# Optimization experiments

Measured on AMD Instinct MI355X. Metric: run time of the kernel, lower is better.

The kernel has to match this reference:

```python
import jax, jax.numpy as jnp
import numpy as np

NODE, HIDDEN, BATCH, OUT, BUF = 200, 10, 50, 64, 500
DT = 0.0001
# ParamsJR('JR') defaults (all variances 0 -> constants, not Parameters)
A_, a_, B_, b_ = 3.25, 100.0, 22.0, 50.0
g_, c1_, c2_, c3_, c4_ = 1000.0, 135.0, 135.0 * 0.8, 135.0 * 0.25, 135.0 * 0.25
std_in_, vmax, v0, r_, y0, cy0 = 100.0, 5.0, 6.0, 0.56, 2.0, 5.0
LB, U_UB, NOISE_LB, SAT = 0.01, 500.0, 150.0, 1000.0


def setup_inputs() -> dict:
    key = jax.random.key(0)
    ks = jax.random.split(key, 8)
    inp = jax.random.normal(ks[0], (NODE, HIDDEN, BATCH), dtype=jnp.float32)
    noise_in = jax.random.normal(ks[1], (NODE, HIDDEN, BATCH), dtype=jnp.float32)
    hx = jax.random.uniform(ks[2], (NODE, 6), dtype=jnp.float32)
    hE = jax.random.uniform(ks[3], (NODE, BUF), dtype=jnp.float32)
    sc = jax.random.uniform(ks[4], (NODE, NODE), dtype=jnp.float32)
    w_bb = jax.random.uniform(ks[5], (NODE, NODE), dtype=jnp.float32)  # fitted gains (init 0.05 in torch)
    lm = jax.random.normal(ks[6], (OUT, NODE), dtype=jnp.float32)  # lead-field
    delays = jax.random.randint(ks[7], (NODE, NODE), 0, BUF)  # (dist/(1.5+relu(mu))).int64
    return {"inp": inp, "noise_in": noise_in, "hx": hx, "hE": hE,
            "sc": sc, "w_bb": w_bb, "lm": lm, "delays": delays}


def _sigmoid(x):
    return vmax / (1.0 + jnp.exp(r_ * (v0 - x)))


def _sys2nd(A, a, u, x, v):
    return A * a * u - 2.0 * a * v - a * a * x


def _forward(inp, noise_in, hx, hE, sc, w_bb, lm, delays):
    relu = jax.nn.relu
    A_e, a_e = relu(A_), 1.0 + relu(a_)          # 0*con+relu(A), 1*con+relu(a)
    B_e, b_e = relu(B_), 1.0 + relu(b_)
    g_e, c1e, c2e, c3e, c4e = (LB + relu(g_), LB + relu(c1_), LB + relu(c2_),
                               LB + relu(c3_), LB + relu(c4_))
    std_e = NOISE_LB + relu(std_in_)

    # normalized laplacian-style connectivity
    w = jnp.exp(w_bb) * sc
    wl = jnp.log1p(0.5 * (w + w.T))
    w_n = wl / jnp.linalg.norm(wl)
    dg = -jnp.diag(jnp.sum(w_n, axis=1))          # (node, node)
    rows = jnp.arange(NODE)[:, None]

    def step(carry, xs):
        M, E, I, Mv, Ev, Iv, hEb = carry
        u, noise = xs                              # (node,1) each
        Ed = hEb[rows, delays]                     # Ed[i,j] = hE[i, delays[i,j]]
        LEd = jnp.sum(w_n * Ed.T, axis=1, keepdims=True)  # (node,1)
        rM = _sigmoid(E - I)
        rE = (std_e * noise + g_e * (LEd + dg @ E)
              + c2e * _sigmoid(c1e * M))
        rI = c4e * _sigmoid(c3e * M)
        ddM = M + DT * Mv
        ddE = E + DT * Ev
        ddI = I + DT * Iv
        ddMv = Mv + DT * _sys2nd(A_e, a_e, u + U_UB * jnp.tanh(rM / U_UB), M, Mv)
        ddEv = Ev + DT * _sys2nd(A_e, a_e, U_UB * jnp.tanh(rE / U_UB), E, Ev)
        ddIv = Iv + DT * _sys2nd(B_e, b_e, U_UB * jnp.tanh(rI / U_UB), I, Iv)
        sat = lambda x: SAT * jnp.tanh(x / SAT)
        M, E, I, Mv, Ev, Iv = (sat(ddM), sat(ddE), sat(ddI),
                               sat(ddMv), sat(ddEv), sat(ddIv))
        hEb = jnp.concatenate([M, hEb[:, :-1]], axis=1)  # push pyramidal state into delay buffer
        return (M, E, I, Mv, Ev, Iv, hEb), None

    def tr_step(carry, xs):
        u_tr, n_tr = xs                            # (hidden, node, 1)
        carry, _ = jax.lax.scan(step, carry, (u_tr, n_tr))
        M, E, I, Mv, Ev, Iv, _ = carry
        return carry, (M[:, 0], E[:, 0], I[:, 0], Mv[:, 0], Ev[:, 0], Iv[:, 0])

    M, E, I = hx[:, 0:1], hx[:, 1:2], hx[:, 2:3]
    Mv, Ev, Iv = hx[:, 3:4], hx[:, 4:5], hx[:, 5:6]
    u_all = jnp.transpose(inp, (2, 1, 0))[..., None]       # (batch, hidden, node, 1)
    n_all = jnp.transpose(noise_in, (2, 1, 0))[..., None]
    carry, recs = jax.lax.scan(tr_step, (M, E, I, Mv, Ev, Iv, hE), (u_all, n_all))
    Mb, Eb, Ib, Mvb, Evb, Ivb = recs                       # (batch, node) each

    # lead-field: row-normalize then remove channel mean
    lm_n = lm / jnp.sqrt(jnp.sum(lm ** 2, axis=1, keepdims=True))
    lm_t = lm_n - jnp.mean(lm_n, axis=0, keepdims=True)
    eeg = cy0 * jnp.einsum('on,bn->ob', lm_t, Eb - Ib) - y0  # (output, batch)

    M, E, I, Mv, Ev, Iv, hEb = carry
    current_state = jnp.concatenate([M, E, I, Mv, Ev, Iv], axis=1)
    return eeg, current_state, Eb.T, Ib.T, Mb.T, Evb.T, Ivb.T, Mvb.T, hEb


def reference(inp, noise_in, hx, hE, sc, w_bb, lm, delays):
    return _forward(inp, noise_in, hx, hE, sc, w_bb, lm, delays)
```

## Files before the change

kernel.cpp:

```cpp
#include <hip/hip_runtime.h>
#include <math.h>

#define N_NODE 200
#define RING   512
#define ROWF   545
#define NSTEP  500
#define TB     32
#define NB     16
#define NWG    8
#define NTHR   256
#define JSL    25
#define NEARCAP 32
#define MDEP   36

#define FPBUF   (NWG * N_NODE * TB)
#define OFF_FP  0
#define OFF_BAR (2 * FPBUF)
#define WS_NEED ((size_t)(2 * FPBUF + 64) * 4)

#define SM_RED   0
#define SM_MREC  64
#define SM_US    28864
#define SM_NS    54464
#define SM_LED   80864
#define SM_RING  106464
#define SM_TOTAL 160964
#define SM_LMT   64
#define SM_DIFF  51264

__device__ __forceinline__ float ftanh(float x) {
    float ax = fabsf(x);
    float t  = __expf(-2.0f * ax);
    float r  = __fdividef(1.0f - t, 1.0f + t);
    return copysignf(r, x);
}
__device__ __forceinline__ float sigm(float x) {
    return __fdividef(5.0f, 1.0f + __expf(0.56f * (6.0f - x)));
}
__device__ __forceinline__ float satf(float x) {
    return 1000.0f * ftanh(x * 0.001f);
}

__device__ __forceinline__ void grid_barrier(int* slot, int nwg) {
    __syncthreads();
    if (threadIdx.x == 0) {
        __threadfence();
        __hip_atomic_fetch_add(slot, 1, __ATOMIC_ACQ_REL, __HIP_MEMORY_SCOPE_AGENT);
        while (__hip_atomic_load(slot, __ATOMIC_ACQUIRE, __HIP_MEMORY_SCOPE_AGENT) < nwg) {
            __builtin_amdgcn_s_sleep(2);
        }
        __threadfence();
    }
    __syncthreads();
}

__global__ void zero_bar(int* bar) {
    if (threadIdx.x < 64) bar[threadIdx.x] = 0;
}

__global__ __launch_bounds__(NTHR, 1)
void jansen_fast(const float* __restrict__ inp, const float* __restrict__ noise_in,
                 const float* __restrict__ hx,  const float* __restrict__ hE,
                 const float* __restrict__ sc,  const float* __restrict__ wbb,
                 const float* __restrict__ lm,  const int*   __restrict__ delays,
                 float* __restrict__ out, float* __restrict__ ws)
{
    __shared__ char smem[SM_TOTAL];
    double*   red  = (double*)(smem + SM_RED);
    float*    Mrec = (float*)(smem + SM_MREC);
    unsigned* nOFF = (unsigned*)(smem + SM_US);
    float*    nW   = (float*)(smem + SM_NS);
    float*    uS   = (float*)(smem + SM_US);
    float*    nS   = (float*)(smem + SM_NS);
    float*    LEdS = (float*)(smem + SM_LED);
    float*    ringS= (float*)(smem + SM_RING);

    const int tid = threadIdx.x;
    const int wg  = blockIdx.x;
    const int i   = tid;
    const int jlo = wg * JSL;

    float* fp  = ws + OFF_FP;
    int*   bar = (int*)(ws + OFF_BAR);

    double ssq = 0.0;
    for (int q = tid; q < N_NODE * N_NODE; q += NTHR) {
        int j = q / N_NODE, ii = q - j * N_NODE;
        float w1 = expf(wbb[ii * N_NODE + j]) * sc[ii * N_NODE + j];
        float w2 = expf(wbb[j * N_NODE + ii]) * sc[j * N_NODE + ii];
        float wl = log1pf(0.5f * (w1 + w2));
        ssq += (double)wl * (double)wl;
    }
    #pragma unroll
    for (int off = 32; off > 0; off >>= 1) ssq += __shfl_down(ssq, off, 64);
    if ((tid & 63) == 0) red[tid >> 6] = ssq;

    for (int p = tid; p < JSL * ROWF; p += NTHR) {
        int jl = p / ROWF, x = p - jl * ROWF;
        float v = 0.0f;
        if (x < 544) {
            int dd = (x < RING) ? (511 - x) : (1023 - x);
            if (dd < 500) v = hE[(jlo + jl) * 500 + dd];
        }
        ringS[p] = v;
    }
    for (int p = tid; p < MDEP * N_NODE; p += NTHR) {
        int s = p / N_NODE, j = p - s * N_NODE;
        Mrec[p] = (s >= 4) ? hE[j * 500 + (35 - s)] : 0.0f;
    }
    for (int p = tid; p < NEARCAP * N_NODE; p += NTHR) {
        nOFF[p] = 0u;
        nW[p]   = 0.0f;
    }
    __syncthreads();
    if (tid == 0) {
        double s = 0.0;
        #pragma unroll
        for (int r = 0; r < 8; ++r) s += red[r];
        red[0] = 1.0 / sqrt(s);
    }
    __syncthreads();
    const float inv = (float)red[0];

    float rowsum = 0.0f;
    float M = 0, E = 0, I = 0, Mvv = 0, Evv = 0, Ivv = 0;
    float wreg[JSL];
    int   ereg[JSL];
    #pragma unroll
    for (int jl = 0; jl < JSL; ++jl) { wreg[jl] = 0.0f; ereg[jl] = 0; }
    if (i < N_NODE) {
        int cnt = 0;
        for (int j = 0; j < N_NODE; ++j) {
            float w1 = expf(wbb[i * N_NODE + j]) * sc[i * N_NODE + j];
            float w2 = expf(wbb[j * N_NODE + i]) * sc[j * N_NODE + i];
            float w  = log1pf(0.5f * (w1 + w2)) * inv;
            int d = delays[j * N_NODE + i];
            rowsum += w;
            if (d < NEARCAP && cnt < NEARCAP) {
                nOFF[cnt * N_NODE + i] = (unsigned)((35 - d) * N_NODE + j);
                nW  [cnt * N_NODE + i] = w;
                ++cnt;
            }
        }
        #pragma unroll
        for (int jl = 0; jl < JSL; ++jl) {
            int j = jlo + jl;
            float w1 = expf(wbb[i * N_NODE + j]) * sc[i * N_NODE + j];
            float w2 = expf(wbb[j * N_NODE + i]) * sc[j * N_NODE + i];
            float w  = log1pf(0.5f * (w1 + w2)) * inv;
            int d = delays[j * N_NODE + i];
            wreg[jl] = (d < NEARCAP) ? 0.0f : w;
            ereg[jl] = 511 - d;
        }
        M   = hx[i * 6 + 0]; E   = hx[i * 6 + 1]; I   = hx[i * 6 + 2];
        Mvv = hx[i * 6 + 3]; Evv = hx[i * 6 + 4]; Ivv = hx[i * 6 + 5];
    }

    int   noffR[NEARCAP];
    float nwR[NEARCAP];
    {
        const int ii = (i < N_NODE) ? i : 0;
        #pragma unroll
        for (int n = 0; n < NEARCAP; ++n) {
            noffR[n] = (int)nOFF[n * N_NODE + ii];
            nwR[n]   = nW[n * N_NODE + ii];
        }
    }
    __syncthreads();

    for (int b = 0; b < NB; ++b) {
        const int t0 = b * TB;
        float* fpb = fp + (b & 1) * FPBUF;

        if (i < N_NODE) {
            float ac[TB];
            #pragma unroll
            for (int k = 0; k < TB; ++k) ac[k] = 0.0f;
            #pragma unroll
            for (int jl = 0; jl < JSL; ++jl) {
                float w  = wreg[jl];
                int   p0 = (t0 + ereg[jl]) & 511;
                const float* rb = ringS + jl * ROWF + p0;
                #pragma unroll
                for (int k = 0; k < TB; ++k)
                    ac[k] = fmaf(w, rb[k], ac[k]);
            }
            float4* fpw = (float4*)(fpb + wg * (N_NODE * TB) + i * TB);
            #pragma unroll
            for (int q = 0; q < 8; ++q)
                fpw[q] = make_float4(ac[4*q+0], ac[4*q+1], ac[4*q+2], ac[4*q+3]);

            #pragma unroll
            for (int k = 0; k < TB; ++k) {
                int t = t0 + k;
                float uv = 0.0f, nv = 0.0f;
                if (t < NSTEP) {
                    int bb = t / 10, h = t - 10 * bb;
                    uv = inp     [i * 500 + h * 50 + bb];
                    nv = noise_in[i * 500 + h * 50 + bb];
                }
                uS[k * N_NODE + i] = uv;
                nS[k * N_NODE + i] = nv;
            }
        }

        grid_barrier(bar + b, NWG);

        if (i < N_NODE) {
            const float* basep = fpb + i * TB;
            #pragma unroll
            for (int c = 0; c < 8; ++c) {
                float sx = 0, sy = 0, sz = 0, sw = 0;
                #pragma unroll
                for (int g = 0; g < NWG; ++g) {
                    float4 q = *(const float4*)(basep + g * (N_NODE * TB) + c * 4);
                    sx += q.x; sy += q.y; sz += q.z; sw += q.w;
                }
                LEdS[(c * 4 + 0) * N_NODE + i] = sx;
                LEdS[(c * 4 + 1) * N_NODE + i] = sy;
                LEdS[(c * 4 + 2) * N_NODE + i] = sz;
                LEdS[(c * 4 + 3) * N_NODE + i] = sw;
            }
        }
        __syncthreads();

        const int kmax = (NSTEP - t0 < TB) ? (NSTEP - t0) : TB;
        int s36 = t0 % MDEP;
        int bcur = t0 / 10, hcur = t0 - 10 * bcur;
        const bool ringw = (i >= jlo) && (i < jlo + JSL);
        const int  rbase = (i - jlo) * ROWF;
        for (int k = 0; k < kmax; ++k) {
            const int t = t0 + k;
            if (i < N_NODE) {
                const int base36 = s36 * N_NODE;
                float a0 = LEdS[k * N_NODE + i];
                float a1 = 0.0f, a2 = 0.0f, a3 = 0.0f;
                #pragma unroll
                for (int n = 0; n < NEARCAP; n += 4) {
                    int d0 = base36 + noffR[n+0]; if (d0 >= MDEP*N_NODE) d0 -= MDEP*N_NODE;
                    int d1 = base36 + noffR[n+1]; if (d1 >= MDEP*N_NODE) d1 -= MDEP*N_NODE;
                    int d2 = base36 + noffR[n+2]; if (d2 >= MDEP*N_NODE) d2 -= MDEP*N_NODE;
                    int d3 = base36 + noffR[n+3]; if (d3 >= MDEP*N_NODE) d3 -= MDEP*N_NODE;
                    a0 = fmaf(nwR[n+0], Mrec[d0], a0);
                    a1 = fmaf(nwR[n+1], Mrec[d1], a1);
                    a2 = fmaf(nwR[n+2], Mrec[d2], a2);
                    a3 = fmaf(nwR[n+3], Mrec[d3], a3);
                }
                float LEd = (a0 + a1) + (a2 + a3);
                float u  = uS[k * N_NODE + i];
                float nz = nS[k * N_NODE + i];
                float rM = sigm(E - I);
                float rE = 250.0f * nz + 1000.01f * (LEd - rowsum * E) + 108.01f * sigm(135.01f * M);
                float rI = 33.76f * sigm(33.76f * M);
                float ddM = M + 1e-4f * Mvv;
                float ddE = E + 1e-4f * Evv;
                float ddI = I + 1e-4f * Ivv;
                float uu  = u + 500.0f * ftanh(rM * 0.002f);
                float ddMv = Mvv + 1e-4f * (328.25f * uu - 202.0f * Mvv - 10201.0f * M);
                float uE  = 500.0f * ftanh(rE * 0.002f);
                float ddEv = Evv + 1e-4f * (328.25f * uE - 202.0f * Evv - 10201.0f * E);
                float uI  = 500.0f * ftanh(rI * 0.002f);
                float ddIv = Ivv + 1e-4f * (1122.0f * uI - 102.0f * Ivv - 2601.0f * I);
                M   = satf(ddM);  E   = satf(ddE);  I   = satf(ddI);
                Mvv = satf(ddMv); Evv = satf(ddEv); Ivv = satf(ddIv);
                Mrec[base36 + i] = M;
                if (ringw) {
                    int pt = t & 511;
                    ringS[rbase + pt] = M;
                    if (pt < 32) ringS[rbase + pt + 512] = M;
                }
                if (wg == 0 && hcur == 9) {
                    out[ 4400 + i * 50 + bcur] = E;
                    out[14400 + i * 50 + bcur] = I;
                    out[24400 + i * 50 + bcur] = M;
                    out[34400 + i * 50 + bcur] = Evv;
                    out[44400 + i * 50 + bcur] = Ivv;
                    out[54400 + i * 50 + bcur] = Mvv;
                }
                ++hcur; if (hcur == 10) { hcur = 0; ++bcur; }
                ++s36; if (s36 == MDEP) s36 = 0;
            }
            __syncthreads();
        }
    }

    for (int p = tid; p < JSL * 500; p += NTHR) {
        int jl = p / 500, dd = p - jl * 500;
        out[64400 + (jlo + jl) * 500 + dd] = ringS[jl * ROWF + ((499 - dd) & 511)];
    }
    if (wg != 0) return;

    if (i < N_NODE) {
        out[3200 + i * 6 + 0] = M;
        out[3200 + i * 6 + 1] = E;
        out[3200 + i * 6 + 2] = I;
        out[3200 + i * 6 + 3] = Mvv;
        out[3200 + i * 6 + 4] = Evv;
        out[3200 + i * 6 + 5] = Ivv;
    }

    float* lmt  = (float*)(smem + SM_LMT);
    float* diff = (float*)(smem + SM_DIFF);
    __syncthreads();
    if (tid < 64) {
        float s = 0.0f;
        for (int n = 0; n < N_NODE; ++n) { float v = lm[tid * N_NODE + n]; s += v * v; }
        float ivn = 1.0f / sqrtf(s);
        for (int n = 0; n < N_NODE; ++n) lmt[tid * N_NODE + n] = lm[tid * N_NODE + n] * ivn;
    }
    __syncthreads();
    if (tid < N_NODE) {
        float s = 0.0f;
        for (int o = 0; o < 64; ++o) s += lmt[o * N_NODE + tid];
        s *= (1.0f / 64.0f);
        for (int o = 0; o < 64; ++o) lmt[o * N_NODE + tid] -= s;
    }
    __syncthreads();
    for (int p = tid; p < 10000; p += NTHR) diff[p] = out[4400 + p] - out[14400 + p];
    __syncthreads();
    for (int p = tid; p < 3200; p += NTHR) {
        int o = p / 50, bb = p - o * 50;
        float s = 0.0f;
        for (int n = 0; n < N_NODE; ++n)
            s = fmaf(lmt[o * N_NODE + n], diff[n * 50 + bb], s);
        out[p] = 5.0f * s - 2.0f;
    }
}

__global__ __launch_bounds__(1024, 1)
void jansen_main(const float* __restrict__ inp, const float* __restrict__ noise_in,
                 const float* __restrict__ hx,  const float* __restrict__ hE,
                 const float* __restrict__ sc,  const float* __restrict__ wbb,
                 const float* __restrict__ lm,  const int*   __restrict__ delays,
                 float* __restrict__ out, float* __restrict__ ws)
{
    const int tid = threadIdx.x;
    const int i   = tid & 255;
    const int c   = tid >> 8;

    float* ring = ws;
    float* lmt  = ws + N_NODE * RING;

    __shared__ double red[18];
    __shared__ float  part[4][N_NODE];
    __shared__ float  wn[N_NODE * N_NODE];

    double ssq = 0.0;
    for (int p = tid; p < N_NODE * N_NODE; p += 1024) {
        int r0 = p / N_NODE;
        int cc = p - r0 * N_NODE;
        float w1 = expf(wbb[p]) * sc[p];
        float w2 = expf(wbb[cc * N_NODE + r0]) * sc[cc * N_NODE + r0];
        float v  = log1pf(0.5f * (w1 + w2));
        wn[p] = v;
        ssq += (double)v * (double)v;
    }
    #pragma unroll
    for (int off = 32; off > 0; off >>= 1) ssq += __shfl_down(ssq, off, 64);
    if ((tid & 63) == 0) red[tid >> 6] = ssq;
    __syncthreads();
    if (tid == 0) {
        double s = 0.0;
        for (int k = 0; k < 16; ++k) s += red[k];
        red[16] = 1.0 / sqrt(s);
    }
    __syncthreads();
    const float inv_norm = (float)red[16];
    for (int p = tid; p < N_NODE * N_NODE; p += 1024) wn[p] *= inv_norm;

    for (int p = tid; p < N_NODE * 500; p += 1024) {
        int j = p / 500, dd = p - j * 500;
        ring[j * RING + (511 - dd)] = hE[p];
    }
    if (tid < 64) {
        float s = 0.0f;
        for (int n = 0; n < N_NODE; ++n) { float v = lm[tid * N_NODE + n]; s += v * v; }
        float inv = 1.0f / sqrtf(s);
        for (int n = 0; n < N_NODE; ++n) lmt[tid * N_NODE + n] = lm[tid * N_NODE + n] * inv;
    }
    __syncthreads();
    if (tid < N_NODE) {
        float s = 0.0f;
        for (int o = 0; o < 64; ++o) s += lmt[o * N_NODE + tid];
        s *= (1.0f / 64.0f);
        for (int o = 0; o < 64; ++o) lmt[o * N_NODE + tid] -= s;
    }

    unsigned int dpk[25];
    if (i < N_NODE) {
        #pragma unroll
        for (int r0 = 0; r0 < 25; ++r0) {
            int d0 = delays[(c * 50 + 2 * r0    ) * N_NODE + i];
            int d1 = delays[(c * 50 + 2 * r0 + 1) * N_NODE + i];
            unsigned e0 = (unsigned)((-1 - d0) & 511);
            unsigned e1 = (unsigned)((-1 - d1) & 511);
            dpk[r0] = e0 | (e1 << 16);
        }
    }

    float M = 0, E = 0, I = 0, Mvv = 0, Evv = 0, Ivv = 0, rowsum = 0;
    if (c == 0 && i < N_NODE) {
        M   = hx[i * 6 + 0]; E   = hx[i * 6 + 1]; I   = hx[i * 6 + 2];
        Mvv = hx[i * 6 + 3]; Evv = hx[i * 6 + 4]; Ivv = hx[i * 6 + 5];
    }
    __syncthreads();
    if (c == 0 && i < N_NODE) {
        float s = 0.0f;
        for (int j = 0; j < N_NODE; ++j) s += wn[j * N_NODE + i];
        rowsum = s;
    }

    for (int t = 0; t < NSTEP; ++t) {
        if (i < N_NODE) {
            float acc = 0.0f;
            const float* ringc = ring + c * 50 * RING;
            const float* wnc   = wn + c * 50 * N_NODE + i;
            #pragma unroll
            for (int r0 = 0; r0 < 50; ++r0) {
                unsigned e = (dpk[r0 >> 1] >> ((r0 & 1) << 4)) & 0xffffu;
                int pos = (int)(((unsigned)t + e) & 511u);
                acc = fmaf(wnc[r0 * N_NODE], ringc[r0 * RING + pos], acc);
            }
            part[c][i] = acc;
        }
        __syncthreads();
        if (c == 0 && i < N_NODE) {
            float LEd = part[0][i] + part[1][i] + part[2][i] + part[3][i];
            int b = t / 10, h = t - b * 10;
            float u  = inp     [i * 500 + h * 50 + b];
            float nz = noise_in[i * 500 + h * 50 + b];
            float rM = 5.0f / (1.0f + expf(0.56f * (6.0f - (E - I))));
            float rE = 250.0f * nz + 1000.01f * (LEd - rowsum * E) + 108.01f * (5.0f / (1.0f + expf(0.56f * (6.0f - 135.01f * M))));
            float rI = 33.76f * (5.0f / (1.0f + expf(0.56f * (6.0f - 33.76f * M))));
            float ddM = M + 1e-4f * Mvv;
            float ddE = E + 1e-4f * Evv;
            float ddI = I + 1e-4f * Ivv;
            float uu  = u + 500.0f * tanhf(rM / 500.0f);
            float ddMv = Mvv + 1e-4f * (328.25f * uu - 202.0f * Mvv - 10201.0f * M);
            float uE  = 500.0f * tanhf(rE / 500.0f);
            float ddEv = Evv + 1e-4f * (328.25f * uE - 202.0f * Evv - 10201.0f * E);
            float uI  = 500.0f * tanhf(rI / 500.0f);
            float ddIv = Ivv + 1e-4f * (1122.0f * uI - 102.0f * Ivv - 2601.0f * I);
            M   = 1000.0f * tanhf(ddM / 1000.0f);
            E   = 1000.0f * tanhf(ddE / 1000.0f);
            I   = 1000.0f * tanhf(ddI / 1000.0f);
            Mvv = 1000.0f * tanhf(ddMv / 1000.0f);
            Evv = 1000.0f * tanhf(ddEv / 1000.0f);
            Ivv = 1000.0f * tanhf(ddIv / 1000.0f);
            ring[i * RING + (t & 511)] = M;
            if (h == 9) {
                out[ 4400 + i * 50 + b] = E;
                out[14400 + i * 50 + b] = I;
                out[24400 + i * 50 + b] = M;
                out[34400 + i * 50 + b] = Evv;
                out[44400 + i * 50 + b] = Ivv;
                out[54400 + i * 50 + b] = Mvv;
            }
        }
        __syncthreads();
    }

    if (c == 0 && i < N_NODE) {
        out[3200 + i * 6 + 0] = M;
        out[3200 + i * 6 + 1] = E;
        out[3200 + i * 6 + 2] = I;
        out[3200 + i * 6 + 3] = Mvv;
        out[3200 + i * 6 + 4] = Evv;
        out[3200 + i * 6 + 5] = Ivv;
    }
    for (int p = tid; p < N_NODE * 500; p += 1024) {
        int ii = p / 500, dd = p - ii * 500;
        out[64400 + p] = ring[ii * RING + (499 - dd)];
    }
    __syncthreads();
    for (int p = tid; p < 64 * 50; p += 1024) {
        int o = p / 50, b = p - o * 50;
        float s = 0.0f;
        for (int n = 0; n < N_NODE; ++n)
            s += lmt[o * N_NODE + n] * (out[4400 + n * 50 + b] - out[14400 + n * 50 + b]);
        out[p] = 5.0f * s - 2.0f;
    }
}

extern "C" void kernel_launch(void* const* d_in, const int* in_sizes, int n_in,
                              void* d_out, int out_size, void* d_ws, size_t ws_size,
                              hipStream_t stream) {
    if (ws_size >= WS_NEED) {
        zero_bar<<<1, 64, 0, stream>>>((int*)((float*)d_ws + OFF_BAR));
        jansen_fast<<<NWG, NTHR, 0, stream>>>(
            (const float*)d_in[0], (const float*)d_in[1], (const float*)d_in[2],
            (const float*)d_in[3], (const float*)d_in[4], (const float*)d_in[5],
            (const float*)d_in[6], (const int*)d_in[7],
            (float*)d_out, (float*)d_ws);
    } else {
        jansen_main<<<1, 1024, 0, stream>>>(
            (const float*)d_in[0], (const float*)d_in[1], (const float*)d_in[2],
            (const float*)d_in[3], (const float*)d_in[4], (const float*)d_in[5],
            (const float*)d_in[6], (const int*)d_in[7],
            (float*)d_out, (float*)d_ws);
    }
}
```

Baseline: 1.210 ms.

## Run sequential inner recurrence in a single wavefront with four nodes per lane

The per-step recurrence is moved from 200 threads synchronised with __syncthreads every step to one 64-lane wavefront, where each lane owns four nodes and the block barriers inside the time loop are dropped. The near-delay window shrinks from 32 to 16 steps, so more connections go through the blocked far-field accumulation, and the time block is halved from 32 to 16 steps, which doubles the number of grid barriers. Near-neighbour sums use variable-length chunks based on per-node counts. The intent is to remove per-step workgroup barrier cost at the expense of four times more serial arithmetic per lane.

```diff
diff --git a/kernel.cpp b/kernel.cpp
--- a/kernel.cpp
+++ b/kernel.cpp
@@ -3,15 +3,17 @@
 
 #define N_NODE 200
 #define RING   512
-#define ROWF   545
+#define ROWF   527
 #define NSTEP  500
-#define TB     32
-#define NB     16
+#define TB     16
+#define NB     32
 #define NWG    8
 #define NTHR   256
 #define JSL    25
-#define NEARCAP 32
-#define MDEP   36
+#define NEARB  16
+#define NCAP   24
+#define MDEP   20
+#define MSZ    (MDEP * N_NODE)
 
 #define FPBUF   (NWG * N_NODE * TB)
 #define OFF_FP  0
@@ -20,11 +22,14 @@
 
 #define SM_RED   0
 #define SM_MREC  64
-#define SM_US    28864
-#define SM_NS    54464
-#define SM_LED   80864
-#define SM_RING  106464
-#define SM_TOTAL 160964
+#define SM_LEDS  16064
+#define SM_UN    28864
+#define SM_NCNT  54464
+#define SM_ST    55264
+#define SM_RING  91264
+#define SM_TOTAL 143964
+#define SM_NX    16064
+#define SM_NW2   35264
 #define SM_LMT   64
 #define SM_DIFF  51264
 
@@ -59,21 +64,22 @@
 }
 
 __global__ __launch_bounds__(NTHR, 1)
-void jansen_fast(const float* __restrict__ inp, const float* __restrict__ noise_in,
-                 const float* __restrict__ hx,  const float* __restrict__ hE,
-                 const float* __restrict__ sc,  const float* __restrict__ wbb,
-                 const float* __restrict__ lm,  const int*   __restrict__ delays,
-                 float* __restrict__ out, float* __restrict__ ws)
+void jansen_1w(const float* __restrict__ inp, const float* __restrict__ noise_in,
+               const float* __restrict__ hx,  const float* __restrict__ hE,
+               const float* __restrict__ sc,  const float* __restrict__ wbb,
+               const float* __restrict__ lm,  const int*   __restrict__ delays,
+               float* __restrict__ out, float* __restrict__ ws)
 {
     __shared__ char smem[SM_TOTAL];
     double*   red  = (double*)(smem + SM_RED);
-    float*    Mrec = (float*)(smem + SM_MREC);
-    unsigned* nOFF = (unsigned*)(smem + SM_US);
-    float*    nW   = (float*)(smem + SM_NS);
-    float*    uS   = (float*)(smem + SM_US);
-    float*    nS   = (float*)(smem + SM_NS);
-    float*    LEdS = (float*)(smem + SM_LED);
+    float*    MrecF= (float*)(smem + SM_MREC);
+    float*    LEdS = (float*)(smem + SM_LEDS);
+    float*    unF  = (float*)(smem + SM_UN);
+    unsigned* nCnt = (unsigned*)(smem + SM_NCNT);
+    float*    stS  = (float*)(smem + SM_ST);
     float*    ringS= (float*)(smem + SM_RING);
+    unsigned* nX   = (unsigned*)(smem + SM_NX);
+    float*    nW2  = (float*)(smem + SM_NW2);
 
     const int tid = threadIdx.x;
     const int wg  = blockIdx.x;
@@ -97,38 +103,28 @@
 
     for (int p = tid; p < JSL * ROWF; p += NTHR) {
         int jl = p / ROWF, x = p - jl * ROWF;
-        float v = 0.0f;
-        if (x < 544) {
-            int dd = (x < RING) ? (511 - x) : (1023 - x);
-            if (dd < 500) v = hE[(jlo + jl) * 500 + dd];
-        }
-        ringS[p] = v;
-    }
-    for (int p = tid; p < MDEP * N_NODE; p += NTHR) {
+        int dd = (x < RING) ? (511 - x) : (1023 - x);
+        ringS[p] = (dd < 500) ? hE[(jlo + jl) * 500 + dd] : 0.0f;
+    }
+    for (int p = tid; p < MSZ; p += NTHR) {
         int s = p / N_NODE, j = p - s * N_NODE;
-        Mrec[p] = (s >= 4) ? hE[j * 500 + (35 - s)] : 0.0f;
-    }
-    for (int p = tid; p < NEARCAP * N_NODE; p += NTHR) {
-        nOFF[p] = 0u;
-        nW[p]   = 0.0f;
-    }
+        MrecF[p] = (s >= 4) ? hE[j * 500 + (19 - s)] : 0.0f;
+    }
+    for (int p = tid; p < NCAP * N_NODE; p += NTHR) { nX[p] = 0u; nW2[p] = 0.0f; }
     __syncthreads();
     if (tid == 0) {
-        double s = 0.0;
-        #pragma unroll
-        for (int r = 0; r < 8; ++r) s += red[r];
+        double s = red[0] + red[1] + red[2] + red[3];
         red[0] = 1.0 / sqrt(s);
     }
     __syncthreads();
     const float inv = (float)red[0];
 
-    float rowsum = 0.0f;
-    float M = 0, E = 0, I = 0, Mvv = 0, Evv = 0, Ivv = 0;
     float wreg[JSL];
     int   ereg[JSL];
     #pragma unroll
     for (int jl = 0; jl < JSL; ++jl) { wreg[jl] = 0.0f; ereg[jl] = 0; }
     if (i < N_NODE) {
+        float rowsum = 0.0f;
         int cnt = 0;
         for (int j = 0; j < N_NODE; ++j) {
             float w1 = expf(wbb[i * N_NODE + j]) * sc[i * N_NODE + j];
@@ -136,12 +132,13 @@
             float w  = log1pf(0.5f * (w1 + w2)) * inv;
             int d = delays[j * N_NODE + i];
             rowsum += w;
-            if (d < NEARCAP && cnt < NEARCAP) {
-                nOFF[cnt * N_NODE + i] = (unsigned)((35 - d) * N_NODE + j);
-                nW  [cnt * N_NODE + i] = w;
+            if (d < NEARB && cnt < NCAP) {
+                nX [cnt * N_NODE + i] = (unsigned)((19 - d) * N_NODE + j);
+                nW2[cnt * N_NODE + i] = w;
                 ++cnt;
             }
         }
+        nCnt[i] = (unsigned)cnt;
         #pragma unroll
         for (int jl = 0; jl < JSL; ++jl) {
             int j = jlo + jl;
@@ -149,22 +146,53 @@
             float w2 = expf(wbb[j * N_NODE + i]) * sc[j * N_NODE + i];
             float w  = log1pf(0.5f * (w1 + w2)) * inv;
             int d = delays[j * N_NODE + i];
-            wreg[jl] = (d < NEARCAP) ? 0.0f : w;
+            wreg[jl] = (d < NEARB) ? 0.0f : w;
             ereg[jl] = 511 - d;
         }
-        M   = hx[i * 6 + 0]; E   = hx[i * 6 + 1]; I   = hx[i * 6 + 2];
-        Mvv = hx[i * 6 + 3]; Evv = hx[i * 6 + 4]; Ivv = hx[i * 6 + 5];
-    }
-
-    int   noffR[NEARCAP];
-    float nwR[NEARCAP];
-    {
-        const int ii = (i < N_NODE) ? i : 0;
+        stS[0 * N_NODE + i] = hx[i * 6 + 0];
+        stS[1 * N_NODE + i] = hx[i * 6 + 1];
+        stS[2 * N_NODE + i] = hx[i * 6 + 2];
+        stS[3 * N_NODE + i] = hx[i * 6 + 3];
+        stS[4 * N_NODE + i] = hx[i * 6 + 4];
+        stS[5 * N_NODE + i] = hx[i * 6 + 5];
+        stS[6 * N_NODE + i] = rowsum;
+    }
+    __syncthreads();
+
+    const int  nb        = tid * 4;
+    const bool innerLane = (tid < 64) && (nb < N_NODE);
+    int   pkA[4 * NCAP]; float wkA[4 * NCAP];
+    int   cq[4];
+    float Mq[4] = {0,0,0,0}, Eq[4] = {0,0,0,0}, Iq[4] = {0,0,0,0};
+    float Mvq[4] = {0,0,0,0}, Evq[4] = {0,0,0,0}, Ivq[4] = {0,0,0,0};
+    float rsq[4] = {0,0,0,0};
+    #pragma unroll
+    for (int z = 0; z < 4 * NCAP; ++z) { pkA[z] = 0; wkA[z] = 0.0f; }
+    cq[0] = cq[1] = cq[2] = cq[3] = 0;
+    if (innerLane) {
         #pragma unroll
-        for (int n = 0; n < NEARCAP; ++n) {
-            noffR[n] = (int)nOFF[n * N_NODE + ii];
-            nwR[n]   = nW[n * N_NODE + ii];
-        }
+        for (int q = 0; q < 4; ++q) {
+            cq[q] = (int)nCnt[nb + q];
+            #pragma unroll
+            for (int n = 0; n < NCAP; ++n) {
+                pkA[q * NCAP + n] = (int)nX[n * N_NODE + nb + q];
+                wkA[q * NCAP + n] = nW2[n * N_NODE + nb + q];
+            }
+        }
+        float4 v0 = *(const float4*)(stS + 0 * N_NODE + nb);
+        float4 v1 = *(const float4*)(stS + 1 * N_NODE + nb);
+        float4 v2 = *(const float4*)(stS + 2 * N_NODE + nb);
+        float4 v3 = *(const float4*)(stS + 3 * N_NODE + nb);
+        float4 v4 = *(const float4*)(stS + 4 * N_NODE + nb);
+        float4 v5 = *(const float4*)(stS + 5 * N_NODE + nb);
+        float4 v6 = *(const float4*)(stS + 6 * N_NODE + nb);
+        Mq[0]=v0.x; Mq[1]=v0.y; Mq[2]=v0.z; Mq[3]=v0.w;
+        Eq[0]=v1.x; Eq[1]=v1.y; Eq[2]=v1.z; Eq[3]=v1.w;
+        Iq[0]=v2.x; Iq[1]=v2.y; Iq[2]=v2.z; Iq[3]=v2.w;
+        Mvq[0]=v3.x; Mvq[1]=v3.y; Mvq[2]=v3.z; Mvq[3]=v3.w;
+        Evq[0]=v4.x; Evq[1]=v4.y; Evq[2]=v4.z; Evq[3]=v4.w;
+        Ivq[0]=v5.x; Ivq[1]=v5.y; Ivq[2]=v5.z; Ivq[3]=v5.w;
+        rsq[0]=v6.x; rsq[1]=v6.y; rsq[2]=v6.z; rsq[3]=v6.w;
     }
     __syncthreads();
 
@@ -187,7 +215,7 @@
             }
             float4* fpw = (float4*)(fpb + wg * (N_NODE * TB) + i * TB);
             #pragma unroll
-            for (int q = 0; q < 8; ++q)
+            for (int q = 0; q < 4; ++q)
                 fpw[q] = make_float4(ac[4*q+0], ac[4*q+1], ac[4*q+2], ac[4*q+3]);
 
             #pragma unroll
@@ -199,89 +227,109 @@
                     uv = inp     [i * 500 + h * 50 + bb];
                     nv = noise_in[i * 500 + h * 50 + bb];
                 }
-                uS[k * N_NODE + i] = uv;
-                nS[k * N_NODE + i] = nv;
+                ((float2*)unF)[k * N_NODE + i] = make_float2(uv, nv);
             }
         }
 
         grid_barrier(bar + b, NWG);
 
         if (i < N_NODE) {
-            const float* basep = fpb + i * TB;
-            #pragma unroll
-            for (int c = 0; c < 8; ++c) {
-                float sx = 0, sy = 0, sz = 0, sw = 0;
+            float sA[TB];
+            #pragma unroll
+            for (int k = 0; k < TB; ++k) sA[k] = 0.0f;
+            #pragma unroll
+            for (int g = 0; g < NWG; ++g) {
+                const float4* row = (const float4*)(fpb + g * (N_NODE * TB) + i * TB);
                 #pragma unroll
-                for (int g = 0; g < NWG; ++g) {
-                    float4 q = *(const float4*)(basep + g * (N_NODE * TB) + c * 4);
-                    sx += q.x; sy += q.y; sz += q.z; sw += q.w;
+                for (int c = 0; c < 4; ++c) {
+                    float4 qv = row[c];
+                    sA[4*c+0] += qv.x; sA[4*c+1] += qv.y;
+                    sA[4*c+2] += qv.z; sA[4*c+3] += qv.w;
                 }
-                LEdS[(c * 4 + 0) * N_NODE + i] = sx;
-                LEdS[(c * 4 + 1) * N_NODE + i] = sy;
-                LEdS[(c * 4 + 2) * N_NODE + i] = sz;
-                LEdS[(c * 4 + 3) * N_NODE + i] = sw;
-            }
+            }
+            #pragma unroll
+            for (int k = 0; k < TB; ++k) LEdS[k * N_NODE + i] = sA[k];
         }
         __syncthreads();
 
-        const int kmax = (NSTEP - t0 < TB) ? (NSTEP - t0) : TB;
-        int s36 = t0 % MDEP;
-        int bcur = t0 / 10, hcur = t0 - 10 * bcur;
-        const bool ringw = (i >= jlo) && (i < jlo + JSL);
-        const int  rbase = (i - jlo) * ROWF;
-        for (int k = 0; k < kmax; ++k) {
-            const int t = t0 + k;
-            if (i < N_NODE) {
-                const int base36 = s36 * N_NODE;
-                float a0 = LEdS[k * N_NODE + i];
-                float a1 = 0.0f, a2 = 0.0f, a3 = 0.0f;
+        if (innerLane) {
+            const int kmax = (NSTEP - t0 < TB) ? (NSTEP - t0) : TB;
+            int s200 = (t0 % MDEP) * N_NODE;
+            int bcur = t0 / 10, hcur = t0 - 10 * bcur;
+            for (int k = 0; k < kmax; ++k) {
+                const float4 led4 = *(const float4*)(LEdS + k * N_NODE + nb);
+                const float4 unA  = *(const float4*)(unF + 2 * (k * N_NODE + nb));
+                const float4 unB  = *(const float4*)(unF + 2 * (k * N_NODE + nb) + 4);
+                float led[4] = {led4.x, led4.y, led4.z, led4.w};
+                float uq[4]  = {unA.x, unA.z, unB.x, unB.z};
+                float nq[4]  = {unA.y, unA.w, unB.y, unB.w};
                 #pragma unroll
-                for (int n = 0; n < NEARCAP; n += 4) {
-                    int d0 = base36 + noffR[n+0]; if (d0 >= MDEP*N_NODE) d0 -= MDEP*N_NODE;
-                    int d1 = base36 + noffR[n+1]; if (d1 >= MDEP*N_NODE) d1 -= MDEP*N_NODE;
-                    int d2 = base36 + noffR[n+2]; if (d2 >= MDEP*N_NODE) d2 -= MDEP*N_NODE;
-                    int d3 = base36 + noffR[n+3]; if (d3 >= MDEP*N_NODE) d3 -= MDEP*N_NODE;
-                    a0 = fmaf(nwR[n+0], Mrec[d0], a0);
-                    a1 = fmaf(nwR[n+1], Mrec[d1], a1);
-                    a2 = fmaf(nwR[n+2], Mrec[d2], a2);
-                    a3 = fmaf(nwR[n+3], Mrec[d3], a3);
+                for (int q = 0; q < 4; ++q) {
+                    float LEd = led[q];
+                    const int qb = q * NCAP;
+                    #pragma unroll
+                    for (int n = 0; n < 8; ++n) {
+                        int a = s200 + pkA[qb + n]; if (a >= MSZ) a -= MSZ;
+                        LEd = fmaf(wkA[qb + n], MrecF[a], LEd);
+                    }
+                    if (cq[q] > 8) {
+                        #pragma unroll
+                        for (int n = 8; n < 16; ++n) {
+                            int a = s200 + pkA[qb + n]; if (a >= MSZ) a -= MSZ;
+                            LEd = fmaf(wkA[qb + n], MrecF[a], LEd);
+                        }
+                    }
+                    if (cq[q] > 16) {
+                        #pragma unroll
+                        for (int n = 16; n < 24; ++n) {
+                            int a = s200 + pkA[qb + n]; if (a >= MSZ) a -= MSZ;
+                            LEd = fmaf(wkA[qb + n], MrecF[a], LEd);
+                        }
+                    }
+                    float rM = sigm(Eq[q] - Iq[q]);
+                    float rE = 250.0f * nq[q] + 1000.01f * (LEd - rsq[q] * Eq[q]) + 108.01f * sigm(135.01f * Mq[q]);
+                    float rI = 33.76f * sigm(33.76f * Mq[q]);
+                    float ddM = Mq[q] + 1e-4f * Mvq[q];
+                    float ddE = Eq[q] + 1e-4f * Evq[q];
+                    float ddI = Iq[q] + 1e-4f * Ivq[q];
+                    float uu  = uq[q] + 500.0f * ftanh(rM * 0.002f);
+                    float ddMv = Mvq[q] + 1e-4f * (328.25f * uu - 202.0f * Mvq[q] - 10201.0f * Mq[q]);
+                    float uE  = 500.0f * ftanh(rE * 0.002f);
+                    float ddEv = Evq[q] + 1e-4f * (328.25f * uE - 202.0f * Evq[q] - 10201.0f * Eq[q]);
+                    float uI  = 500.0f * ftanh(rI * 0.002f);
+                    float ddIv = Ivq[q] + 1e-4f * (1122.0f * uI - 102.0f * Ivq[q] - 2601.0f * Iq[q]);
+                    Mq[q]  = satf(ddM);  Eq[q]  = satf(ddE);  Iq[q]  = satf(ddI);
+                    Mvq[q] = satf(ddMv); Evq[q] = satf(ddEv); Ivq[q] = satf(ddIv);
                 }
-                float LEd = (a0 + a1) + (a2 + a3);
-                float u  = uS[k * N_NODE + i];
-                float nz = nS[k * N_NODE + i];
-                float rM = sigm(E - I);
-                float rE = 250.0f * nz + 1000.01f * (LEd - rowsum * E) + 108.01f * sigm(135.01f * M);
-                float rI = 33.76f * sigm(33.76f * M);
-                float ddM = M + 1e-4f * Mvv;
-                float ddE = E + 1e-4f * Evv;
-                float ddI = I + 1e-4f * Ivv;
-                float uu  = u + 500.0f * ftanh(rM * 0.002f);
-                float ddMv = Mvv + 1e-4f * (328.25f * uu - 202.0f * Mvv - 10201.0f * M);
-                float uE  = 500.0f * ftanh(rE * 0.002f);
-                float ddEv = Evv + 1e-4f * (328.25f * uE - 202.0f * Evv - 10201.0f * E);
-                float uI  = 500.0f * ftanh(rI * 0.002f);
-                float ddIv = Ivv + 1e-4f * (1122.0f * uI - 102.0f * Ivv - 2601.0f * I);
-                M   = satf(ddM);  E   = satf(ddE);  I   = satf(ddI);
-                Mvv = satf(ddMv); Evv = satf(ddEv); Ivv = satf(ddIv);
-                Mrec[base36 + i] = M;
-                if (ringw) {
-                    int pt = t & 511;
-                    ringS[rbase + pt] = M;
-                    if (pt < 32) ringS[rbase + pt + 512] = M;
+                *(float4*)(MrecF + s200 + nb) = make_float4(Mq[0], Mq[1], Mq[2], Mq[3]);
+                const int t = t0 + k;
+                const int pt = t & 511;
+                #pragma unroll
+                for (int q = 0; q < 4; ++q) {
+                    int nd = nb + q;
+                    if (nd >= jlo && nd < jlo + JSL) {
+                        int rb2 = (nd - jlo) * ROWF;
+                        ringS[rb2 + pt] = Mq[q];
+                        if (pt < 15) ringS[rb2 + pt + 512] = Mq[q];
+                    }
                 }
                 if (wg == 0 && hcur == 9) {
-                    out[ 4400 + i * 50 + bcur] = E;
-                    out[14400 + i * 50 + bcur] = I;
-                    out[24400 + i * 50 + bcur] = M;
-                    out[34400 + i * 50 + bcur] = Evv;
-                    out[44400 + i * 50 + bcur] = Ivv;
-                    out[54400 + i * 50 + bcur] = Mvv;
+                    #pragma unroll
+                    for (int q = 0; q < 4; ++q) {
+                        int nd = nb + q;
+                        out[ 4400 + nd * 50 + bcur] = Eq[q];
+                        out[14400 + nd * 50 + bcur] = Iq[q];
+                        out[24400 + nd * 50 + bcur] = Mq[q];
+                        out[34400 + nd * 50 + bcur] = Evq[q];
+                        out[44400 + nd * 50 + bcur] = Ivq[q];
+                        out[54400 + nd * 50 + bcur] = Mvq[q];
+                    }
                 }
                 ++hcur; if (hcur == 10) { hcur = 0; ++bcur; }
-                ++s36; if (s36 == MDEP) s36 = 0;
-            }
-            __syncthreads();
-        }
+                s200 += N_NODE; if (s200 == MSZ) s200 = 0;
+            }
+        }
+        __syncthreads();
     }
 
     for (int p = tid; p < JSL * 500; p += NTHR) {
@@ -290,13 +338,17 @@
     }
     if (wg != 0) return;
 
-    if (i < N_NODE) {
-        out[3200 + i * 6 + 0] = M;
-        out[3200 + i * 6 + 1] = E;
-        out[3200 + i * 6 + 2] = I;
-        out[3200 + i * 6 + 3] = Mvv;
-        out[3200 + i * 6 + 4] = Evv;
-        out[3200 + i * 6 + 5] = Ivv;
+    if (innerLane) {
+        #pragma unroll
+        for (int q = 0; q < 4; ++q) {
+            int nd = nb + q;
+            out[3200 + nd * 6 + 0] = Mq[q];
+            out[3200 + nd * 6 + 1] = Eq[q];
+            out[3200 + nd * 6 + 2] = Iq[q];
+            out[3200 + nd * 6 + 3] = Mvq[q];
+            out[3200 + nd * 6 + 4] = Evq[q];
+            out[3200 + nd * 6 + 5] = Ivq[q];
+        }
     }
 
     float* lmt  = (float*)(smem + SM_LMT);
@@ -487,7 +539,7 @@
                               hipStream_t stream) {
     if (ws_size >= WS_NEED) {
         zero_bar<<<1, 64, 0, stream>>>((int*)((float*)d_ws + OFF_BAR));
-        jansen_fast<<<NWG, NTHR, 0, stream>>>(
+        jansen_1w<<<NWG, NTHR, 0, stream>>>(
             (const float*)d_in[0], (const float*)d_in[1], (const float*)d_in[2],
             (const float*)d_in[3], (const float*)d_in[4], (const float*)d_in[5],
             (const float*)d_in[6], (const int*)d_in[7],
```

New measurement: 3.014 ms. +149.0%, slower.

## Split each workgroup into two thread teams for far-delay accumulation

Applied to the files above, without the earlier changes.

Doubles threads per workgroup and splits the far-delay j-slice between two 256-thread teams. Each team writes its own partial-sum buffer, and the reducer sums 16 partials. The serial recurrence is duplicated in both teams, with only team 0 writing shared state. It also packs u/noise into float2 and skips near-delay groups beyond each node's count. This aims to cut per-thread register pressure and the latency of the parallel accumulation, at the cost of redundant serial compute, double partial-buffer traffic and a larger reduction.

```diff
diff --git a/kernel.cpp b/kernel.cpp
--- a/kernel.cpp
+++ b/kernel.cpp
@@ -8,23 +8,26 @@
 #define TB     32
 #define NB     16
 #define NWG    8
-#define NTHR   256
+#define NTHR   512
 #define JSL    25
+#define TJ0    13
 #define NEARCAP 32
 #define MDEP   36
-
-#define FPBUF   (NWG * N_NODE * TB)
+#define MSZ    (MDEP * N_NODE)
+
+#define FPBUF   (2 * NWG * N_NODE * TB)
 #define OFF_FP  0
 #define OFF_BAR (2 * FPBUF)
 #define WS_NEED ((size_t)(2 * FPBUF + 64) * 4)
 
 #define SM_RED   0
 #define SM_MREC  64
-#define SM_US    28864
-#define SM_NS    54464
-#define SM_LED   80864
-#define SM_RING  106464
-#define SM_TOTAL 160964
+#define SM_UN    28864
+#define SM_LEDS  80064
+#define SM_RING  105664
+#define SM_TOTAL 160164
+#define SM_NOFF  SM_UN
+#define SM_NW    (SM_UN + 25600)
 #define SM_LMT   64
 #define SM_DIFF  51264
 
@@ -58,27 +61,29 @@
     if (threadIdx.x < 64) bar[threadIdx.x] = 0;
 }
 
-__global__ __launch_bounds__(NTHR, 1)
-void jansen_fast(const float* __restrict__ inp, const float* __restrict__ noise_in,
-                 const float* __restrict__ hx,  const float* __restrict__ hE,
-                 const float* __restrict__ sc,  const float* __restrict__ wbb,
-                 const float* __restrict__ lm,  const int*   __restrict__ delays,
-                 float* __restrict__ out, float* __restrict__ ws)
+__global__ __launch_bounds__(NTHR, 2)
+void jansen_tlp(const float* __restrict__ inp, const float* __restrict__ noise_in,
+                const float* __restrict__ hx,  const float* __restrict__ hE,
+                const float* __restrict__ sc,  const float* __restrict__ wbb,
+                const float* __restrict__ lm,  const int*   __restrict__ delays,
+                float* __restrict__ out, float* __restrict__ ws)
 {
     __shared__ char smem[SM_TOTAL];
     double*   red  = (double*)(smem + SM_RED);
     float*    Mrec = (float*)(smem + SM_MREC);
-    unsigned* nOFF = (unsigned*)(smem + SM_US);
-    float*    nW   = (float*)(smem + SM_NS);
-    float*    uS   = (float*)(smem + SM_US);
-    float*    nS   = (float*)(smem + SM_NS);
-    float*    LEdS = (float*)(smem + SM_LED);
+    unsigned* nOFF = (unsigned*)(smem + SM_NOFF);
+    float*    nW   = (float*)(smem + SM_NW);
+    float2*   unS  = (float2*)(smem + SM_UN);
+    float*    LEdS = (float*)(smem + SM_LEDS);
     float*    ringS= (float*)(smem + SM_RING);
 
-    const int tid = threadIdx.x;
-    const int wg  = blockIdx.x;
-    const int i   = tid;
-    const int jlo = wg * JSL;
+    const int tid   = threadIdx.x;
+    const int wg    = blockIdx.x;
+    const int team  = tid >> 8;
+    const int i     = tid & 255;
+    const int jlo_w = wg * JSL;
+    const int jlo_t = jlo_w + team * TJ0;
+    const int jcnt  = team ? (JSL - TJ0) : TJ0;
 
     float* fp  = ws + OFF_FP;
     int*   bar = (int*)(ws + OFF_BAR);
@@ -100,11 +105,11 @@
         float v = 0.0f;
         if (x < 544) {
             int dd = (x < RING) ? (511 - x) : (1023 - x);
-            if (dd < 500) v = hE[(jlo + jl) * 500 + dd];
+            if (dd < 500) v = hE[(jlo_w + jl) * 500 + dd];
         }
         ringS[p] = v;
     }
-    for (int p = tid; p < MDEP * N_NODE; p += NTHR) {
+    for (int p = tid; p < MSZ; p += NTHR) {
         int s = p / N_NODE, j = p - s * N_NODE;
         Mrec[p] = (s >= 4) ? hE[j * 500 + (35 - s)] : 0.0f;
     }
@@ -124,12 +129,12 @@
 
     float rowsum = 0.0f;
     float M = 0, E = 0, I = 0, Mvv = 0, Evv = 0, Ivv = 0;
-    float wreg[JSL];
-    int   ereg[JSL];
+    float wreg[TJ0];
+    int   ereg[TJ0];
     #pragma unroll
-    for (int jl = 0; jl < JSL; ++jl) { wreg[jl] = 0.0f; ereg[jl] = 0; }
+    for (int jl = 0; jl < TJ0; ++jl) { wreg[jl] = 0.0f; ereg[jl] = 511; }
+    int cnt = 0;
     if (i < N_NODE) {
-        int cnt = 0;
         for (int j = 0; j < N_NODE; ++j) {
             float w1 = expf(wbb[i * N_NODE + j]) * sc[i * N_NODE + j];
             float w2 = expf(wbb[j * N_NODE + i]) * sc[j * N_NODE + i];
@@ -143,14 +148,16 @@
             }
         }
         #pragma unroll
-        for (int jl = 0; jl < JSL; ++jl) {
-            int j = jlo + jl;
-            float w1 = expf(wbb[i * N_NODE + j]) * sc[i * N_NODE + j];
-            float w2 = expf(wbb[j * N_NODE + i]) * sc[j * N_NODE + i];
-            float w  = log1pf(0.5f * (w1 + w2)) * inv;
-            int d = delays[j * N_NODE + i];
-            wreg[jl] = (d < NEARCAP) ? 0.0f : w;
-            ereg[jl] = 511 - d;
+        for (int jl = 0; jl < TJ0; ++jl) {
+            if (jl < jcnt) {
+                int j = jlo_t + jl;
+                float w1 = expf(wbb[i * N_NODE + j]) * sc[i * N_NODE + j];
+                float w2 = expf(wbb[j * N_NODE + i]) * sc[j * N_NODE + i];
+                float w  = log1pf(0.5f * (w1 + w2)) * inv;
+                int d = delays[j * N_NODE + i];
+                wreg[jl] = (d < NEARCAP) ? 0.0f : w;
+                ereg[jl] = 511 - d;
+            }
         }
         M   = hx[i * 6 + 0]; E   = hx[i * 6 + 1]; I   = hx[i * 6 + 2];
         Mvv = hx[i * 6 + 3]; Evv = hx[i * 6 + 4]; Ivv = hx[i * 6 + 5];
@@ -177,21 +184,23 @@
             #pragma unroll
             for (int k = 0; k < TB; ++k) ac[k] = 0.0f;
             #pragma unroll
-            for (int jl = 0; jl < JSL; ++jl) {
+            for (int jl = 0; jl < TJ0; ++jl) {
                 float w  = wreg[jl];
                 int   p0 = (t0 + ereg[jl]) & 511;
-                const float* rb = ringS + jl * ROWF + p0;
+                int   lr = team * TJ0 + jl; if (lr > 24) lr = 24;
+                const float* rb = ringS + lr * ROWF + p0;
                 #pragma unroll
                 for (int k = 0; k < TB; ++k)
                     ac[k] = fmaf(w, rb[k], ac[k]);
             }
-            float4* fpw = (float4*)(fpb + wg * (N_NODE * TB) + i * TB);
+            float4* fpw = (float4*)(fpb + ((wg * 2 + team) * N_NODE + i) * TB);
             #pragma unroll
             for (int q = 0; q < 8; ++q)
                 fpw[q] = make_float4(ac[4*q+0], ac[4*q+1], ac[4*q+2], ac[4*q+3]);
 
             #pragma unroll
-            for (int k = 0; k < TB; ++k) {
+            for (int k2 = 0; k2 < 16; ++k2) {
+                int k = team * 16 + k2;
                 int t = t0 + k;
                 float uv = 0.0f, nv = 0.0f;
                 if (t < NSTEP) {
@@ -199,8 +208,7 @@
                     uv = inp     [i * 500 + h * 50 + bb];
                     nv = noise_in[i * 500 + h * 50 + bb];
                 }
-                uS[k * N_NODE + i] = uv;
-                nS[k * N_NODE + i] = nv;
+                unS[k * N_NODE + i] = make_float2(uv, nv);
             }
         }
 
@@ -209,10 +217,11 @@
         if (i < N_NODE) {
             const float* basep = fpb + i * TB;
             #pragma unroll
-            for (int c = 0; c < 8; ++c) {
+            for (int c2 = 0; c2 < 4; ++c2) {
+                int c = (team << 2) + c2;
                 float sx = 0, sy = 0, sz = 0, sw = 0;
                 #pragma unroll
-                for (int g = 0; g < NWG; ++g) {
+                for (int g = 0; g < 2 * NWG; ++g) {
                     float4 q = *(const float4*)(basep + g * (N_NODE * TB) + c * 4);
                     sx += q.x; sy += q.y; sz += q.z; sw += q.w;
                 }
@@ -227,8 +236,8 @@
         const int kmax = (NSTEP - t0 < TB) ? (NSTEP - t0) : TB;
         int s36 = t0 % MDEP;
         int bcur = t0 / 10, hcur = t0 - 10 * bcur;
-        const bool ringw = (i >= jlo) && (i < jlo + JSL);
-        const int  rbase = (i - jlo) * ROWF;
+        const bool ringw = (i >= jlo_t) && (i < jlo_t + jcnt);
+        const int  rbase = (i - jlo_w) * ROWF;
         for (int k = 0; k < kmax; ++k) {
             const int t = t0 + k;
             if (i < N_NODE) {
@@ -236,19 +245,35 @@
                 float a0 = LEdS[k * N_NODE + i];
                 float a1 = 0.0f, a2 = 0.0f, a3 = 0.0f;
                 #pragma unroll
-                for (int n = 0; n < NEARCAP; n += 4) {
-                    int d0 = base36 + noffR[n+0]; if (d0 >= MDEP*N_NODE) d0 -= MDEP*N_NODE;
-                    int d1 = base36 + noffR[n+1]; if (d1 >= MDEP*N_NODE) d1 -= MDEP*N_NODE;
-                    int d2 = base36 + noffR[n+2]; if (d2 >= MDEP*N_NODE) d2 -= MDEP*N_NODE;
-                    int d3 = base36 + noffR[n+3]; if (d3 >= MDEP*N_NODE) d3 -= MDEP*N_NODE;
-                    a0 = fmaf(nwR[n+0], Mrec[d0], a0);
-                    a1 = fmaf(nwR[n+1], Mrec[d1], a1);
-                    a2 = fmaf(nwR[n+2], Mrec[d2], a2);
-                    a3 = fmaf(nwR[n+3], Mrec[d3], a3);
+                for (int n = 0; n < 8; ++n) {
+                    int a = base36 + noffR[n]; if (a >= MSZ) a -= MSZ;
+                    a0 = fmaf(nwR[n], Mrec[a], a0);
+                }
+                if (cnt > 8) {
+                    #pragma unroll
+                    for (int n = 8; n < 16; ++n) {
+                        int a = base36 + noffR[n]; if (a >= MSZ) a -= MSZ;
+                        a1 = fmaf(nwR[n], Mrec[a], a1);
+                    }
+                }
+                if (cnt > 16) {
+                    #pragma unroll
+                    for (int n = 16; n < 24; ++n) {
+                        int a = base36 + noffR[n]; if (a >= MSZ) a -= MSZ;
+                        a2 = fmaf(nwR[n], Mrec[a], a2);
+                    }
+                }
+                if (cnt > 24) {
+                    #pragma unroll
+                    for (int n = 24; n < 32; ++n) {
+                        int a = base36 + noffR[n]; if (a >= MSZ) a -= MSZ;
+                        a3 = fmaf(nwR[n], Mrec[a], a3);
+                    }
                 }
                 float LEd = (a0 + a1) + (a2 + a3);
-                float u  = uS[k * N_NODE + i];
-                float nz = nS[k * N_NODE + i];
+                float2 un = unS[k * N_NODE + i];
+                float u  = un.x;
+                float nz = un.y;
                 float rM = sigm(E - I);
                 float rE = 250.0f * nz + 1000.01f * (LEd - rowsum * E) + 108.01f * sigm(135.01f * M);
                 float rI = 33.76f * sigm(33.76f * M);
@@ -263,13 +288,13 @@
                 float ddIv = Ivv + 1e-4f * (1122.0f * uI - 102.0f * Ivv - 2601.0f * I);
                 M   = satf(ddM);  E   = satf(ddE);  I   = satf(ddI);
                 Mvv = satf(ddMv); Evv = satf(ddEv); Ivv = satf(ddIv);
-                Mrec[base36 + i] = M;
+                if (team == 0) Mrec[base36 + i] = M;
                 if (ringw) {
                     int pt = t & 511;
                     ringS[rbase + pt] = M;
                     if (pt < 32) ringS[rbase + pt + 512] = M;
                 }
-                if (wg == 0 && hcur == 9) {
+                if (team == 0 && wg == 0 && hcur == 9) {
                     out[ 4400 + i * 50 + bcur] = E;
                     out[14400 + i * 50 + bcur] = I;
                     out[24400 + i * 50 + bcur] = M;
@@ -286,11 +311,11 @@
 
     for (int p = tid; p < JSL * 500; p += NTHR) {
         int jl = p / 500, dd = p - jl * 500;
-        out[64400 + (jlo + jl) * 500 + dd] = ringS[jl * ROWF + ((499 - dd) & 511)];
+        out[64400 + (jlo_w + jl) * 500 + dd] = ringS[jl * ROWF + ((499 - dd) & 511)];
     }
     if (wg != 0) return;
 
-    if (i < N_NODE) {
+    if (team == 0 && i < N_NODE) {
         out[3200 + i * 6 + 0] = M;
         out[3200 + i * 6 + 1] = E;
         out[3200 + i * 6 + 2] = I;
@@ -487,7 +512,7 @@
                               hipStream_t stream) {
     if (ws_size >= WS_NEED) {
         zero_bar<<<1, 64, 0, stream>>>((int*)((float*)d_ws + OFF_BAR));
-        jansen_fast<<<NWG, NTHR, 0, stream>>>(
+        jansen_tlp<<<NWG, NTHR, 0, stream>>>(
             (const float*)d_in[0], (const float*)d_in[1], (const float*)d_in[2],
             (const float*)d_in[3], (const float*)d_in[4], (const float*)d_in[5],
             (const float*)d_in[6], (const int*)d_in[7],
```

Result: slower. 1.530 ms (+26.4%).
